# Kernel tuning notes

Measured on AMD Instinct MI355X. Metric: run time of the kernel, lower is better.

## Reference

```python
import jax, jax.numpy as jnp
import numpy as np

B_, L_ = 32, 4096
D_MODEL, D_STATE, D_CONV, EXPAND, N_LAYERS, HORIZON = 128, 16, 4, 2, 4, 1
D_INNER = EXPAND * D_MODEL
DT_RANK = (D_MODEL + 15) // 16  # ceil(d_model/16) = 8
EPS = 1e-6


def setup_inputs() -> dict:
    key = jax.random.key(0)
    ks = jax.random.split(key, 10)
    s = lambda k, sh, sc: jax.random.normal(k, sh, jnp.float32) * sc
    inp = {}
    inp["x"] = s(ks[0], (B_, L_, 1), 1.0)
    inp["input_proj_w"] = s(ks[1], (D_MODEL, 1), 0.5)
    inp["input_proj_b"] = jnp.zeros((D_MODEL,), jnp.float32)
    inp["in_proj_w"] = s(ks[2], (N_LAYERS, 2 * D_INNER, D_MODEL), D_MODEL ** -0.5)
    inp["conv_w"] = s(ks[3], (N_LAYERS, D_INNER, 1, D_CONV), D_CONV ** -0.5)
    inp["conv_b"] = jnp.zeros((N_LAYERS, D_INNER), jnp.float32)
    inp["x_proj_w"] = s(ks[4], (N_LAYERS, DT_RANK + 2 * D_STATE, D_INNER), D_INNER ** -0.5)
    inp["dt_proj_w"] = s(ks[5], (N_LAYERS, D_INNER, DT_RANK), DT_RANK ** -0.5)
    inp["dt_proj_b"] = jnp.full((N_LAYERS, D_INNER), -4.0, jnp.float32)
    inp["A_log"] = jnp.tile(jnp.log(jnp.arange(1, D_STATE + 1, dtype=jnp.float32))[None, None, :], (N_LAYERS, D_INNER, 1))
    inp["D"] = jnp.ones((N_LAYERS, D_INNER), jnp.float32)
    inp["out_proj_w"] = s(ks[6], (N_LAYERS, D_MODEL, D_INNER), D_INNER ** -0.5)
    inp["norm_w"] = jnp.ones((D_MODEL,), jnp.float32)
    inp["output_proj_w"] = s(ks[7], (HORIZON, D_MODEL), D_MODEL ** -0.5)
    inp["output_proj_b"] = jnp.zeros((HORIZON,), jnp.float32)
    return inp


def _mamba_block(h, in_w, cw, cb, xpw, dtw, dtb, alog, d_skip, ow):
    # h: [B, L, d_model] -> [B, L, d_model]
    xz = jnp.einsum('bld,ed->ble', h, in_w)            # [B, L, 2*d_inner]
    x, z = jnp.split(xz, 2, axis=-1)                   # each [B, L, d_inner]
    # depthwise causal conv over time
    xc = jax.lax.conv_general_dilated(
        x.transpose(0, 2, 1), cw, window_strides=(1,),
        padding=[(D_CONV - 1, 0)], feature_group_count=D_INNER,
        dimension_numbers=('NCH', 'OIH', 'NCH'))      # [B, d_inner, L]
    x = jax.nn.silu(xc.transpose(0, 2, 1) + cb)        # [B, L, d_inner]
    dbl = jnp.einsum('blc,ec->ble', x, xpw)            # [B, L, dt_rank+2*d_state]
    dt, Bm, Cm = jnp.split(dbl, [DT_RANK, DT_RANK + D_STATE], axis=-1)
    dt = jax.nn.softplus(jnp.einsum('blr,cr->blc', dt, dtw) + dtb)  # [B, L, d_inner]
    A = -jnp.exp(alog)                                  # [d_inner, d_state]

    def step(hst, inputs):
        dt_t, B_t, C_t, x_t = inputs                   # [B,c],[B,s],[B,s],[B,c]
        hst = jnp.exp(dt_t[..., None] * A) * hst + (dt_t * x_t)[..., None] * B_t[:, None, :]
        y = jnp.einsum('bcs,bs->bc', hst, C_t)
        return hst, y

    h0 = jnp.zeros((x.shape[0], D_INNER, D_STATE), x.dtype)
    xs = (dt.transpose(1, 0, 2), Bm.transpose(1, 0, 2), Cm.transpose(1, 0, 2), x.transpose(1, 0, 2))
    _, ys = jax.lax.scan(step, h0, xs)                 # [L, B, d_inner]
    y = ys.transpose(1, 0, 2) + d_skip * x             # skip: y += D * x
    y = y * jax.nn.silu(z)                             # gating
    return jnp.einsum('blc,dc->bld', y, ow)            # [B, L, d_model]


def reference(x, input_proj_w, input_proj_b, in_proj_w, conv_w, conv_b, x_proj_w,
              dt_proj_w, dt_proj_b, A_log, D, out_proj_w, norm_w,
              output_proj_w, output_proj_b):
    h = jnp.einsum('blo,do->bld', x, input_proj_w) + input_proj_b  # [B, L, d_model]
    for i in range(N_LAYERS):
        h = h + _mamba_block(h, in_proj_w[i], conv_w[i], conv_b[i], x_proj_w[i],
                             dt_proj_w[i], dt_proj_b[i], A_log[i], D[i], out_proj_w[i])
    rms = jnp.sqrt(jnp.mean(h * h, axis=-1, keepdims=True) + EPS)
    h = norm_w * h / rms
    return h[:, -1, :] @ output_proj_w.T + output_proj_b  # [B, horizon]
```

## Files before the change

kernel.cpp:

```cpp
#include <hip/hip_runtime.h>

#define B_    32
#define L_    4096
#define DM    128
#define DI    256
#define DS_   16
#define RANK  8
#define NL    4
#define M_    (B_*L_)
#define NC    64
#define CL    (L_/NC)

typedef __attribute__((ext_vector_type(8))) short short8;
typedef __attribute__((ext_vector_type(4))) float floatx4;
typedef __attribute__((ext_vector_type(2))) float float2v;

__device__ __forceinline__ float b2f(unsigned short u) {
    return __uint_as_float(((unsigned)u) << 16);
}
__device__ __forceinline__ unsigned short f2b(float f) {
    unsigned u = __float_as_uint(f);
    unsigned r = u + 0x7fffu + ((u >> 16) & 1u);
    return (unsigned short)(r >> 16);
}
__device__ __forceinline__ float fast_sig(float v) {
    return __builtin_amdgcn_rcpf(1.f + __expf(-v));
}

__global__ __launch_bounds__(256) void k_detect(const unsigned short* __restrict__ x,
                                                int* __restrict__ flag) {
    __shared__ int cnt;
    if (threadIdx.x == 0) cnt = 0;
    __syncthreads();
    int ok = 0;
    for (int i = 0; i < 4; ++i) {
        unsigned short u = x[threadIdx.x * 4 + i];
        int e = (u >> 7) & 0xFF;
        if ((u & 0x7FFF) == 0 || (e >= 100 && e <= 150)) ok++;
    }
    atomicAdd(&cnt, ok);
    __syncthreads();
    if (threadIdx.x == 0) *flag = (cnt >= 800) ? 1 : 0;
}

struct CvtSeg { const void* src; float* dst; int n; };
struct CvtPack { CvtSeg seg[11]; };
__global__ __launch_bounds__(256) void k_cvt_params(CvtPack p, const int* __restrict__ flag) {
    int s = blockIdx.y;
    int i = blockIdx.x * 256 + threadIdx.x;
    if (i >= p.seg[s].n) return;
    p.seg[s].dst[i] = (*flag) ? b2f(((const unsigned short*)p.seg[s].src)[i])
                              : ((const float*)p.seg[s].src)[i];
}
__global__ __launch_bounds__(256) void k_cvt16(const void* __restrict__ src,
                                               unsigned short* __restrict__ dst,
                                               int n, const int* __restrict__ flag) {
    int i = blockIdx.x * 256 + threadIdx.x;
    if (i >= n) return;
    if (*flag) dst[i] = ((const unsigned short*)src)[i];
    else       dst[i] = f2b(((const float*)src)[i]);
}
__global__ __launch_bounds__(256) void k_xpw48(const void* __restrict__ src,
                                               unsigned short* __restrict__ dst,
                                               const int* __restrict__ flag) {
    int i = blockIdx.x * 256 + threadIdx.x;
    int col = i & 255, rowl = (i >> 8) % 48, layer = i / (48*256);
    unsigned short v = 0;
    if (rowl < 40) {
        int si = (layer*40 + rowl)*256 + col;
        v = (*flag) ? ((const unsigned short*)src)[si] : f2b(((const float*)src)[si]);
    }
    dst[i] = v;
}

__global__ __launch_bounds__(256) void k_init(const void* __restrict__ xraw,
                                              const int* __restrict__ flag,
                                              const float* __restrict__ ipw,
                                              const float* __restrict__ ipb,
                                              float* __restrict__ h, int base) {
    int idx = blockIdx.x * 256 + threadIdx.x;
    int bl = idx >> 7, d = idx & 127;
    float x = (*flag) ? b2f(((const unsigned short*)xraw)[base + bl])
                      : ((const float*)xraw)[base + bl];
    h[idx] = x * ipw[d] + ipb[d];
}

__global__ __launch_bounds__(256) void k_gemm_in(const float* __restrict__ h,
                                                 const unsigned short* __restrict__ w,
                                                 unsigned short* __restrict__ xb,
                                                 unsigned short* __restrict__ zb) {
    __shared__ unsigned short lA[64][136];
    __shared__ unsigned short lW[256][40];
    int tid = threadIdx.x;
    int lane = tid & 63, wv = tid >> 6;
    int ln = lane & 15, qd = lane >> 4;
    int r0 = blockIdx.x * 64;
    int n0 = blockIdx.y * 256;

    {
        int r = tid >> 2;
        int c0 = (tid & 3) * 32;
        const float4* src = (const float4*)(h + (size_t)(r0 + r) * DM + c0);
        for (int j = 0; j < 8; ++j) {
            float4 v = src[j];
            lA[r][c0 + j*4 + 0] = f2b(v.x);
            lA[r][c0 + j*4 + 1] = f2b(v.y);
            lA[r][c0 + j*4 + 2] = f2b(v.z);
            lA[r][c0 + j*4 + 3] = f2b(v.w);
        }
    }

    floatx4 acc[16];
    for (int i = 0; i < 16; ++i) acc[i] = (floatx4)0.f;

    for (int kc = 0; kc < 4; ++kc) {
        __syncthreads();
        {
            int n = tid;
            const uint4* src = (const uint4*)(w + (size_t)(n0 + n) * DM + kc * 32);
            uint4 a = src[0], b = src[1], c = src[2], d = src[3];
            *(uint4*)&lW[n][0]  = a;
            *(uint4*)&lW[n][8]  = b;
            *(uint4*)&lW[n][16] = c;
            *(uint4*)&lW[n][24] = d;
        }
        __syncthreads();
        short8 af = *(const short8*)&lA[wv*16 + ln][kc*32 + qd*8];
        for (int nt = 0; nt < 16; ++nt) {
            short8 bf = *(const short8*)&lW[nt*16 + ln][qd*8];
            acc[nt] = __builtin_amdgcn_mfma_f32_16x16x32_bf16(af, bf, acc[nt], 0, 0, 0);
        }
    }

    for (int nt = 0; nt < 16; ++nt)
        for (int rg = 0; rg < 4; ++rg) {
            size_t gr = (size_t)(r0 + wv*16 + qd*4 + rg);
            int gc = nt*16 + ln;
            unsigned short v = f2b(acc[nt][rg]);
            if (blockIdx.y == 0) xb[gr*DI + gc] = v;
            else                 zb[gr*DI + gc] = v;
        }
}

__device__ __forceinline__ bool a_is_integer_ladder(const float* A) {
    bool f = true;
    #pragma unroll
    for (int s = 0; s < DS_; ++s)
        f = f && (fabsf(A[s] + (float)(s+1)) < 0.01f * (float)(s+1));
    return f;
}

__device__ __forceinline__ void unpack8(uint4 p, float* f) {
    f[0] = b2f((unsigned short)(p.x & 0xffff)); f[1] = b2f((unsigned short)(p.x >> 16));
    f[2] = b2f((unsigned short)(p.y & 0xffff)); f[3] = b2f((unsigned short)(p.y >> 16));
    f[4] = b2f((unsigned short)(p.z & 0xffff)); f[5] = b2f((unsigned short)(p.z >> 16));
    f[6] = b2f((unsigned short)(p.w & 0xffff)); f[7] = b2f((unsigned short)(p.w >> 16));
}
__device__ __forceinline__ void pack16(const float* f, uint4* o) {
    unsigned v[8];
    #pragma unroll
    for (int j = 0; j < 8; ++j)
        v[j] = (unsigned)f2b(f[2*j]) | ((unsigned)f2b(f[2*j+1]) << 16);
    o[0] = make_uint4(v[0], v[1], v[2], v[3]);
    o[1] = make_uint4(v[4], v[5], v[6], v[7]);
}

__global__ __launch_bounds__(256) void k_xprojc(const unsigned short* __restrict__ xb,
                                                const float* __restrict__ cw,
                                                const float* __restrict__ cbp,
                                                const unsigned short* __restrict__ w48,
                                                const float* __restrict__ dtw,
                                                const float* __restrict__ dtb,
                                                const float* __restrict__ alog,
                                                unsigned short* __restrict__ xcg,
                                                unsigned short* __restrict__ dtg,
                                                unsigned short* __restrict__ Bg,
                                                unsigned short* __restrict__ Cg,
                                                unsigned short* __restrict__ Pbuf,
                                                unsigned short* __restrict__ Hbuf) {
    __shared__ unsigned short lA[64][264];
    __shared__ unsigned short lW[48][40];
    __shared__ float ldbl[64][8];
    __shared__ float lBs[64][DS_];
    int tid = threadIdx.x;
    int lane = tid & 63, wv = tid >> 6;
    int ln = lane & 15, qd = lane >> 4;
    int r0 = blockIdx.x * 64;
    int l0 = r0 & (L_ - 1);
    int bidx = r0 >> 12;
    int kidx = l0 >> 6;

    {
        int c = tid;
        float w0 = cw[c*4+0], w1 = cw[c*4+1], w2 = cw[c*4+2], w3 = cw[c*4+3];
        float bias = cbp[c];
        float x0 = (l0 >= 3) ? b2f(xb[(size_t)(r0-3)*DI + c]) : 0.f;
        float x1 = (l0 >= 2) ? b2f(xb[(size_t)(r0-2)*DI + c]) : 0.f;
        float x2 = (l0 >= 1) ? b2f(xb[(size_t)(r0-1)*DI + c]) : 0.f;
        for (int r = 0; r < 64; ++r) {
            float xcur = b2f(xb[(size_t)(r0+r)*DI + c]);
            float v = w0*x0 + w1*x1 + w2*x2 + w3*xcur + bias;
            float s = v * fast_sig(v);
            unsigned short sb = f2b(s);
            lA[r][c] = sb;
            xcg[(size_t)(r0+r)*DI + c] = sb;
            x0 = x1; x1 = x2; x2 = xcur;
        }
    }

    floatx4 acc[3];
    for (int i = 0; i < 3; ++i) acc[i] = (floatx4)0.f;

    for (int kc = 0; kc < 8; ++kc) {
        __syncthreads();
        if (tid < 192) {
            int n = tid >> 2, q = tid & 3;
            *(uint4*)&lW[n][q*8] = *(const uint4*)(w48 + (size_t)n*DI + kc*32 + q*8);
        }
        __syncthreads();
        short8 af = *(const short8*)&lA[wv*16 + ln][kc*32 + qd*8];
        for (int nt = 0; nt < 3; ++nt) {
            short8 bf = *(const short8*)&lW[nt*16 + ln][qd*8];
            acc[nt] = __builtin_amdgcn_mfma_f32_16x16x32_bf16(af, bf, acc[nt], 0, 0, 0);
        }
    }

    for (int nt = 0; nt < 3; ++nt)
        for (int rg = 0; rg < 4; ++rg) {
            int rloc = wv*16 + qd*4 + rg;
            size_t row = (size_t)(r0 + rloc);
            int n = nt*16 + ln;
            float v = acc[nt][rg];
            if (n < 8)       ldbl[rloc][n] = v;
            else if (n < 24) {
                unsigned short bv = f2b(v);
                Bg[row*DS_ + (n-8)] = bv;
                lBs[rloc][n-8] = b2f(bv);
            }
            else if (n < 40) Cg[row*DS_ + (n-24)] = f2b(v);
        }
    __syncthreads();

    {
        int c = tid;
        float w8[8];
        #pragma unroll
        for (int j = 0; j < 8; ++j) w8[j] = dtw[c*8 + j];
        float bias = dtb[c];
        float A[DS_];
        #pragma unroll
        for (int j = 0; j < 4; ++j) {
            float4 a4 = *(const float4*)(alog + c*DS_ + j*4);
            A[j*4+0] = -__expf(a4.x); A[j*4+1] = -__expf(a4.y);
            A[j*4+2] = -__expf(a4.z); A[j*4+3] = -__expf(a4.w);
        }
        float P[DS_], hh[DS_];
        if (a_is_integer_ladder(A)) {
            float2v h2[8];
            #pragma unroll
            for (int j = 0; j < 8; ++j) h2[j] = (float2v)0.f;
            float S = 0.f;
            for (int r = 0; r < 64; ++r) {
                float a = bias;
                #pragma unroll
                for (int j = 0; j < 8; ++j) a += ldbl[r][j] * w8[j];
                float sp = (a > 20.f) ? a : __logf(1.f + __expf(a));
                unsigned short spb = f2b(sp);
                dtg[(size_t)(r0+r)*DI + c] = spb;
                float dtv = b2f(spb);
                float du = dtv * b2f(lA[r][c]);
                float Bl[DS_];
                *(float4*)&Bl[0]  = *(const float4*)&lBs[r][0];
                *(float4*)&Bl[4]  = *(const float4*)&lBs[r][4];
                *(float4*)&Bl[8]  = *(const float4*)&lBs[r][8];
                *(float4*)&Bl[12] = *(const float4*)&lBs[r][12];
                float E = __expf(-dtv);
                float E2 = E * E;
                float2v ep[8];
                ep[0].x = E; ep[0].y = E2;
                float2v E22; E22.x = E2; E22.y = E2;
                #pragma unroll
                for (int j = 1; j < 8; ++j) ep[j] = ep[j-1] * E22;
                float2v du2; du2.x = du; du2.y = du;
                #pragma unroll
                for (int j = 0; j < 8; ++j) {
                    float2v bj; bj.x = Bl[2*j]; bj.y = Bl[2*j+1];
                    h2[j] = ep[j]*h2[j] + du2*bj;
                }
                S += dtv;
            }
            #pragma unroll
            for (int s = 0; s < DS_; ++s) P[s] = __expf(-(float)(s+1) * S);
            #pragma unroll
            for (int j = 0; j < 8; ++j) { hh[2*j] = h2[j].x; hh[2*j+1] = h2[j].y; }
        } else {
            #pragma unroll
            for (int s = 0; s < DS_; ++s) { hh[s] = 0.f; P[s] = 1.f; }
            for (int r = 0; r < 64; ++r) {
                float a = bias;
                #pragma unroll
                for (int j = 0; j < 8; ++j) a += ldbl[r][j] * w8[j];
                float sp = (a > 20.f) ? a : __logf(1.f + __expf(a));
                unsigned short spb = f2b(sp);
                dtg[(size_t)(r0+r)*DI + c] = spb;
                float dtv = b2f(spb);
                float du = dtv * b2f(lA[r][c]);
                float Bl[DS_];
                *(float4*)&Bl[0]  = *(const float4*)&lBs[r][0];
                *(float4*)&Bl[4]  = *(const float4*)&lBs[r][4];
                *(float4*)&Bl[8]  = *(const float4*)&lBs[r][8];
                *(float4*)&Bl[12] = *(const float4*)&lBs[r][12];
                #pragma unroll
                for (int s = 0; s < DS_; ++s) {
                    float e = __expf(dtv * A[s]);
                    hh[s] = e*hh[s] + du*Bl[s];
                    P[s] *= e;
                }
            }
        }
        uint4 op[2], oh[2];
        pack16(P, op);
        pack16(hh, oh);
        uint4* pp = (uint4*)(Pbuf + (((size_t)bidx*NC + kidx)*DI + c)*DS_);
        uint4* ph = (uint4*)(Hbuf + (((size_t)bidx*NC + kidx)*DI + c)*DS_);
        pp[0] = op[0]; pp[1] = op[1];
        ph[0] = oh[0]; ph[1] = oh[1];
    }
}

__global__ __launch_bounds__(256) void k_scan2(const unsigned short* __restrict__ Pbuf,
                                               unsigned short* __restrict__ Hbuf,
                                               int cb) {
    int t = blockIdx.x * 256 + threadIdx.x;
    if (t >= cb * DI * DS_) return;
    int b  = t / (DI * DS_);
    int cs = t % (DI * DS_);
    float H = 0.f;
    for (int k = 0; k < NC; ++k) {
        size_t idx = ((size_t)b * NC + k) * (DI * DS_) + cs;
        float P  = b2f(Pbuf[idx]);
        float he = b2f(Hbuf[idx]);
        Hbuf[idx] = f2b(H);
        H = P * H + he;
    }
}

__global__ __launch_bounds__(256) void k_scan3g(const unsigned short* __restrict__ dtg,
                                                const unsigned short* __restrict__ xcg,
                                                const unsigned short* __restrict__ Bg,
                                                const unsigned short* __restrict__ Cg,
                                                const float* __restrict__ alog,
                                                const unsigned short* __restrict__ Hbuf,
                                                const unsigned short* __restrict__ zb,
                                                const float* __restrict__ Dp,
                                                unsigned short* __restrict__ yg) {
    __shared__ float lB[CL*DS_];
    __shared__ float lC[CL*DS_];
    int c = threadIdx.x;
    int k = blockIdx.x, b = blockIdx.y;
    size_t row0 = (size_t)b * L_ + (size_t)k * CL;
    {
        int t = c & 127;
        const unsigned short* src = (c < 128) ? (Bg + row0*DS_) : (Cg + row0*DS_);
        float* dst = (c < 128) ? lB : lC;
        uint4 p = ((const uint4*)src)[t];
        float f[8]; unpack8(p, f);
        *(float4*)&dst[t*8]     = make_float4(f[0], f[1], f[2], f[3]);
        *(float4*)&dst[t*8 + 4] = make_float4(f[4], f[5], f[6], f[7]);
    }
    float A[DS_];
    #pragma unroll
    for (int j = 0; j < 4; ++j) {
        float4 a4 = *(const float4*)(alog + c*DS_ + j*4);
        A[j*4+0] = -__expf(a4.x); A[j*4+1] = -__expf(a4.y);
        A[j*4+2] = -__expf(a4.z); A[j*4+3] = -__expf(a4.w);
    }
    float Dc = Dp[c];
    float h0[DS_];
    {
        const uint4* ph = (const uint4*)(Hbuf + (((size_t)b*NC + k)*DI + c)*DS_);
        uint4 p0 = ph[0], p1 = ph[1];
        unpack8(p0, &h0[0]);
        unpack8(p1, &h0[8]);
    }
    __syncthreads();
    const unsigned short* pdt = dtg + row0*DI + c;
    const unsigned short* pxc = xcg + row0*DI + c;
    const unsigned short* pz  = zb  + row0*DI + c;
    unsigned short* py        = yg  + row0*DI + c;
    float dtc = b2f(*pdt), xcc = b2f(*pxc), zc = b2f(*pz);

    if (a_is_integer_ladder(A)) {
        float2v h2[8];
        #pragma unroll
        for (int j = 0; j < 8; ++j) { h2[j].x = h0[2*j]; h2[j].y = h0[2*j+1]; }
        for (int l = 0; l < CL; ++l) {
            float dtn = b2f(pdt[DI]); float xcn = b2f(pxc[DI]); float zn = b2f(pz[DI]);
            float du = dtc * xcc;
            float Bl[DS_], Cl[DS_];
            *(float4*)&Bl[0]  = *(const float4*)&lB[l*DS_ + 0];
            *(float4*)&Bl[4]  = *(const float4*)&lB[l*DS_ + 4];
            *(float4*)&Bl[8]  = *(const float4*)&lB[l*DS_ + 8];
            *(float4*)&Bl[12] = *(const float4*)&lB[l*DS_ + 12];
            *(float4*)&Cl[0]  = *(const float4*)&lC[l*DS_ + 0];
            *(float4*)&Cl[4]  = *(const float4*)&lC[l*DS_ + 4];
            *(float4*)&Cl[8]  = *(const float4*)&lC[l*DS_ + 8];
            *(float4*)&Cl[12] = *(const float4*)&lC[l*DS_ + 12];
            float E = __expf(-dtc);
            float E2 = E * E;
            float2v ep[8];
            ep[0].x = E; ep[0].y = E2;
            float2v E22; E22.x = E2; E22.y = E2;
            #pragma unroll
            for (int j = 1; j < 8; ++j) ep[j] = ep[j-1] * E22;
            float2v du2; du2.x = du; du2.y = du;
            float2v y2 = (float2v)0.f;
            #pragma unroll
            for (int j = 0; j < 8; ++j) {
                float2v bj; bj.x = Bl[2*j]; bj.y = Bl[2*j+1];
                float2v cj; cj.x = Cl[2*j]; cj.y = Cl[2*j+1];
                h2[j] = ep[j]*h2[j] + du2*bj;
                y2 = y2 + h2[j]*cj;
            }
            float y = y2.x + y2.y;
            *py = f2b((y + Dc*xcc) * (zc * fast_sig(zc)));
            dtc = dtn; xcc = xcn; zc = zn;
            pdt += DI; pxc += DI; pz += DI; py += DI;
        }
    } else {
        float h[DS_];
        #pragma unroll
        for (int s = 0; s < DS_; ++s) h[s] = h0[s];
        for (int l = 0; l < CL; ++l) {
            float dtn = b2f(pdt[DI]); float xcn = b2f(pxc[DI]); float zn = b2f(pz[DI]);
            float du = dtc * xcc;
            float Bl[DS_], Cl[DS_];
            *(float4*)&Bl[0]  = *(const float4*)&lB[l*DS_ + 0];
            *(float4*)&Bl[4]  = *(const float4*)&lB[l*DS_ + 4];
            *(float4*)&Bl[8]  = *(const float4*)&lB[l*DS_ + 8];
            *(float4*)&Bl[12] = *(const float4*)&lB[l*DS_ + 12];
            *(float4*)&Cl[0]  = *(const float4*)&lC[l*DS_ + 0];
            *(float4*)&Cl[4]  = *(const float4*)&lC[l*DS_ + 4];
            *(float4*)&Cl[8]  = *(const float4*)&lC[l*DS_ + 8];
            *(float4*)&Cl[12] = *(const float4*)&lC[l*DS_ + 12];
            float y = 0.f;
            #pragma unroll
            for (int s = 0; s < DS_; ++s) {
                float e = __expf(dtc * A[s]);
                h[s] = e*h[s] + du*Bl[s];
                y += h[s]*Cl[s];
            }
            *py = f2b((y + Dc*xcc) * (zc * fast_sig(zc)));
            dtc = dtn; xcc = xcn; zc = zn;
            pdt += DI; pxc += DI; pz += DI; py += DI;
        }
    }
}

__global__ __launch_bounds__(256) void k_gemm_oi(const unsigned short* yg,
                                                 const unsigned short* __restrict__ wo,
                                                 const unsigned short* __restrict__ wi,
                                                 float* __restrict__ h,
                                                 unsigned short* xb,
                                                 unsigned short* __restrict__ zb) {
    __shared__ unsigned short lA[64*264];
    __shared__ unsigned short lW[256*40];
    int tid = threadIdx.x;
    int lane = tid & 63, wv = tid >> 6;
    int ln = lane & 15, qd = lane >> 4;
    int r0 = blockIdx.x * 64;

    for (int j = 0; j < 8; ++j) {
        int idx = tid + j*256;
        int r = idx >> 5, q = idx & 31;
        *(uint4*)&lA[r*264 + q*8] = *(const uint4*)(yg + (size_t)(r0 + r)*DI + q*8);
    }
    floatx4 acc1[8];
    for (int i = 0; i < 8; ++i) acc1[i] = (floatx4)0.f;
    for (int kc = 0; kc < 8; ++kc) {
        __syncthreads();
        {
            int n = tid >> 1, half = tid & 1;
            const uint4* src = (const uint4*)(wo + (size_t)n*DI + kc*32 + half*16);
            uint4 a = src[0], b4 = src[1];
            *(uint4*)&lW[n*40 + half*16]     = a;
            *(uint4*)&lW[n*40 + half*16 + 8] = b4;
        }
        __syncthreads();
        short8 af = *(const short8*)&lA[(wv*16 + ln)*264 + kc*32 + qd*8];
        for (int nt = 0; nt < 8; ++nt) {
            short8 bf = *(const short8*)&lW[(nt*16 + ln)*40 + qd*8];
            acc1[nt] = __builtin_amdgcn_mfma_f32_16x16x32_bf16(af, bf, acc1[nt], 0, 0, 0);
        }
    }
    __syncthreads();

    for (int nt = 0; nt < 8; ++nt)
        for (int rg = 0; rg < 4; ++rg) {
            int rloc = wv*16 + qd*4 + rg;
            size_t gr = (size_t)(r0 + rloc);
            int gc = nt*16 + ln;
            float hv = h[gr*DM + gc] + acc1[nt][rg];
            h[gr*DM + gc] = hv;
            lA[rloc*136 + gc] = f2b(hv);
        }
    __syncthreads();

    for (int n0 = 0; n0 < 2; ++n0) {
        floatx4 acc2[16];
        for (int i = 0; i < 16; ++i) acc2[i] = (floatx4)0.f;
        for (int kc = 0; kc < 4; ++kc) {
            __syncthreads();
            {
                int n = tid;
                const uint4* src = (const uint4*)(wi + (size_t)(n0*256 + n)*DM + kc*32);
                uint4 a = src[0], b = src[1], c = src[2], d = src[3];
                *(uint4*)&lW[n*40 + 0]  = a;
                *(uint4*)&lW[n*40 + 8]  = b;
                *(uint4*)&lW[n*40 + 16] = c;
                *(uint4*)&lW[n*40 + 24] = d;
            }
            __syncthreads();
            short8 af = *(const short8*)&lA[(wv*16 + ln)*136 + kc*32 + qd*8];
            for (int nt = 0; nt < 16; ++nt) {
                short8 bf = *(const short8*)&lW[(nt*16 + ln)*40 + qd*8];
                acc2[nt] = __builtin_amdgcn_mfma_f32_16x16x32_bf16(af, bf, acc2[nt], 0, 0, 0);
            }
        }
        unsigned short* dst = (n0 == 0) ? xb : zb;
        for (int nt = 0; nt < 16; ++nt)
            for (int rg = 0; rg < 4; ++rg) {
                size_t gr = (size_t)(r0 + wv*16 + qd*4 + rg);
                int gc = nt*16 + ln;
                dst[gr*DI + gc] = f2b(acc2[nt][rg]);
            }
    }
}

__global__ __launch_bounds__(256) void k_gemm_out(const unsigned short* __restrict__ yg,
                                                  const unsigned short* __restrict__ w,
                                                  float* __restrict__ h) {
    __shared__ unsigned short lA[64][264];
    __shared__ unsigned short lW[128][40];
    int tid = threadIdx.x;
    int lane = tid & 63, wv = tid >> 6;
    int ln = lane & 15, qd = lane >> 4;
    int r0 = blockIdx.x * 64;

    for (int j = 0; j < 8; ++j) {
        int idx = tid + j*256;
        int r = idx >> 5, q = idx & 31;
        *(uint4*)&lA[r][q*8] = *(const uint4*)(yg + (size_t)(r0 + r)*DI + q*8);
    }

    floatx4 acc[8];
    for (int i = 0; i < 8; ++i) acc[i] = (floatx4)0.f;

    for (int kc = 0; kc < 8; ++kc) {
        __syncthreads();
        {
            int n = tid >> 1, half = tid & 1;
            const uint4* src = (const uint4*)(w + (size_t)n*DI + kc*32 + half*16);
            uint4 a = src[0], b4 = src[1];
            *(uint4*)&lW[n][half*16]     = a;
            *(uint4*)&lW[n][half*16 + 8] = b4;
        }
        __syncthreads();
        short8 af = *(const short8*)&lA[wv*16 + ln][kc*32 + qd*8];
        for (int nt = 0; nt < 8; ++nt) {
            short8 bf = *(const short8*)&lW[nt*16 + ln][qd*8];
            acc[nt] = __builtin_amdgcn_mfma_f32_16x16x32_bf16(af, bf, acc[nt], 0, 0, 0);
        }
    }

    for (int nt = 0; nt < 8; ++nt)
        for (int rg = 0; rg < 4; ++rg) {
            size_t gr = (size_t)(r0 + wv*16 + qd*4 + rg);
            int gc = nt*16 + ln;
            h[gr*DM + gc] += acc[nt][rg];
        }
}

__global__ __launch_bounds__(128) void k_head(const float* __restrict__ h,
                                              const float* __restrict__ nw,
                                              const float* __restrict__ opw,
                                              const float* __restrict__ opb,
                                              float* __restrict__ out) {
    __shared__ float red[4];
    int b = blockIdx.x, d = threadIdx.x;
    float hv = h[((size_t)b*L_ + (L_-1))*DM + d];
    float v = hv * hv;
    for (int off = 1; off < 64; off <<= 1) v += __shfl_xor(v, off);
    if ((d & 63) == 0) red[d >> 6] = v;
    __syncthreads();
    float ss = red[0] + red[1];
    float rms = sqrtf(ss * (1.f/DM) + 1e-6f);
    float hn = nw[d] * hv / rms;
    float pv = hn * opw[d];
    for (int off = 1; off < 64; off <<= 1) pv += __shfl_xor(pv, off);
    if ((d & 63) == 0) red[2 + (d >> 6)] = pv;
    __syncthreads();
    if (d == 0) out[b] = red[2] + red[3] + opb[0];
}

extern "C" void kernel_launch(void* const* d_in, const int* in_sizes, int n_in,
                              void* d_out, int out_size, void* d_ws, size_t ws_size,
                              hipStream_t stream) {
    (void)in_sizes; (void)n_in; (void)out_size;
    float* out = (float*)d_out;

    char* wp = (char*)d_ws;
    int* flag = (int*)wp; wp += 16;
    auto allocf = [&](size_t elems) {
        float* p = (float*)wp;
        wp += (elems * 4 + 15) & ~(size_t)15;
        return p;
    };
    auto alloch = [&](size_t elems) {
        unsigned short* p = (unsigned short*)wp;
        wp += (elems * 2 + 15) & ~(size_t)15;
        return p;
    };
    float* c_ipw  = allocf(DM);
    float* c_ipb  = allocf(DM);
    float* c_cw   = allocf((size_t)NL*DI*4);
    float* c_cb   = allocf((size_t)NL*DI);
    float* c_dtw  = allocf((size_t)NL*DI*RANK);
    float* c_dtb  = allocf((size_t)NL*DI);
    float* c_alog = allocf((size_t)NL*DI*DS_);
    float* c_D    = allocf((size_t)NL*DI);
    float* c_nw   = allocf(DM);
    float* c_opw  = allocf(DM);
    float* c_opb  = allocf(1);
    unsigned short* c_inw16 = alloch((size_t)NL*2*DI*DM);
    unsigned short* c_ow16  = alloch((size_t)NL*DM*DI);
    unsigned short* c_xpw48 = alloch((size_t)NL*48*DI);
    wp = (char*)(((size_t)wp + 255) & ~(size_t)255);

    k_detect<<<1, 256, 0, stream>>>((const unsigned short*)d_in[0], flag);

    CvtPack pk;
    pk.seg[0]  = { d_in[1],  c_ipw,  DM };
    pk.seg[1]  = { d_in[2],  c_ipb,  DM };
    pk.seg[2]  = { d_in[4],  c_cw,   NL*DI*4 };
    pk.seg[3]  = { d_in[5],  c_cb,   NL*DI };
    pk.seg[4]  = { d_in[7],  c_dtw,  NL*DI*RANK };
    pk.seg[5]  = { d_in[8],  c_dtb,  NL*DI };
    pk.seg[6]  = { d_in[9],  c_alog, NL*DI*DS_ };
    pk.seg[7]  = { d_in[10], c_D,    NL*DI };
    pk.seg[8]  = { d_in[12], c_nw,   DM };
    pk.seg[9]  = { d_in[13], c_opw,  DM };
    pk.seg[10] = { d_in[14], c_opb,  1 };
    k_cvt_params<<<dim3(64, 11), 256, 0, stream>>>(pk, flag);
    k_cvt16<<<(int)((NL*2*DI*DM + 255)/256), 256, 0, stream>>>(d_in[3],  c_inw16, NL*2*DI*DM, flag);
    k_cvt16<<<(int)((NL*DM*DI   + 255)/256), 256, 0, stream>>>(d_in[11], c_ow16,  NL*DM*DI,   flag);
    k_xpw48<<<NL*48*DI/256, 256, 0, stream>>>(d_in[6], c_xpw48, flag);

    size_t used  = (size_t)(wp - (char*)d_ws);
    size_t avail = (ws_size > used) ? ws_size - used : 0;
    const size_t perB = (size_t)L_ * 2624 + (size_t)2 * NC * DI * DS_ * 2;
    int cb = B_;
    while (cb > 1 && (size_t)cb * perB > avail) cb >>= 1;
    const int Mc = cb * L_;

    float* h            = (float*)wp;          wp += (size_t)Mc*DM*4;
    unsigned short* xb  = (unsigned short*)wp; wp += (size_t)Mc*DI*2;
    unsigned short* zb  = (unsigned short*)wp; wp += (size_t)Mc*DI*2;
    unsigned short* xcg = (unsigned short*)wp; wp += (size_t)Mc*DI*2;
    unsigned short* dty = (unsigned short*)wp; wp += (size_t)Mc*DI*2;
    unsigned short* Bg  = (unsigned short*)wp; wp += (size_t)Mc*DS_*2;
    unsigned short* Cg  = (unsigned short*)wp; wp += (size_t)Mc*DS_*2;
    unsigned short* Pbuf = (unsigned short*)wp; wp += (size_t)cb*NC*DI*DS_*2;
    unsigned short* Hbuf = (unsigned short*)wp; wp += (size_t)cb*NC*DI*DS_*2;

    const int scan2_blocks = (cb * DI * DS_ + 255) / 256;

    for (int b0 = 0; b0 < B_; b0 += cb) {
        k_init<<<Mc*DM/256, 256, 0, stream>>>(d_in[0], flag, c_ipw, c_ipb, h, b0*L_);
        k_gemm_in<<<dim3(Mc/64, 2), 256, 0, stream>>>(h, c_inw16, xb, zb);
        for (int i = 0; i < NL; ++i) {
            k_xprojc<<<Mc/64, 256, 0, stream>>>(xb, c_cw + i*DI*4, c_cb + i*DI,
                                                c_xpw48 + (size_t)i*48*DI,
                                                c_dtw + i*DI*RANK, c_dtb + i*DI,
                                                c_alog + i*DI*DS_,
                                                xcg, dty, Bg, Cg, Pbuf, Hbuf);
            k_scan2<<<scan2_blocks, 256, 0, stream>>>(Pbuf, Hbuf, cb);
            k_scan3g<<<dim3(NC, cb), 256, 0, stream>>>(dty, xcg, Bg, Cg, c_alog + i*DI*DS_,
                                                       Hbuf, zb, c_D + i*DI, xb);
            if (i < NL-1)
                k_gemm_oi<<<Mc/64, 256, 0, stream>>>(xb, c_ow16 + (size_t)i*DM*DI,
                                                     c_inw16 + (size_t)(i+1)*2*DI*DM,
                                                     h, xb, zb);
            else
                k_gemm_out<<<Mc/64, 256, 0, stream>>>(xb, c_ow16 + (size_t)i*DM*DI, h);
        }
        k_head<<<cb, 128, 0, stream>>>(h, c_nw, c_opw, c_opb, out + b0);
    }
}
```

Before: 1.378 ms.

## Compute local scan output in chunk pass and correct with carried state

The first chunked-scan kernel now produces the per-timestep local output y (zero-initial-state contribution) and the cumulative dt sum S, and writes them to global memory instead of dt and B. The third pass no longer reruns the recurrence. It adds the carried-in state contribution analytically, C·exp(A·S)·h0, then applies the skip and gate. This removes the duplicated sequential recurrence in the third pass at the cost of writing two full-width bf16 tensors (yl and S) instead of dt and B, raising memory traffic and workspace. The dt dot product is also vectorised with float2.

New measurement: 1.381 ms. No clear change (+0.2%).

```diff
diff --git a/kernel.cpp b/kernel.cpp
--- a/kernel.cpp
+++ b/kernel.cpp
@@ -173,8 +173,8 @@
                                                 const float* __restrict__ dtb,
                                                 const float* __restrict__ alog,
                                                 unsigned short* __restrict__ xcg,
-                                                unsigned short* __restrict__ dtg,
-                                                unsigned short* __restrict__ Bg,
+                                                unsigned short* __restrict__ ylg,
+                                                unsigned short* __restrict__ Sg,
                                                 unsigned short* __restrict__ Cg,
                                                 unsigned short* __restrict__ Pbuf,
                                                 unsigned short* __restrict__ Hbuf) {
@@ -182,6 +182,7 @@
     __shared__ unsigned short lW[48][40];
     __shared__ float ldbl[64][8];
     __shared__ float lBs[64][DS_];
+    __shared__ float lCs[64][DS_];
     int tid = threadIdx.x;
     int lane = tid & 63, wv = tid >> 6;
     int ln = lane & 15, qd = lane >> 4;
@@ -233,19 +234,21 @@
             float v = acc[nt][rg];
             if (n < 8)       ldbl[rloc][n] = v;
             else if (n < 24) {
-                unsigned short bv = f2b(v);
-                Bg[row*DS_ + (n-8)] = bv;
-                lBs[rloc][n-8] = b2f(bv);
+                lBs[rloc][n-8] = b2f(f2b(v));
             }
-            else if (n < 40) Cg[row*DS_ + (n-24)] = f2b(v);
+            else if (n < 40) {
+                unsigned short cv = f2b(v);
+                Cg[row*DS_ + (n-24)] = cv;
+                lCs[rloc][n-24] = b2f(cv);
+            }
         }
     __syncthreads();
 
     {
         int c = tid;
-        float w8[8];
+        float2v w2v[4];
         #pragma unroll
-        for (int j = 0; j < 8; ++j) w8[j] = dtw[c*8 + j];
+        for (int j = 0; j < 4; ++j) { w2v[j].x = dtw[c*8 + 2*j]; w2v[j].y = dtw[c*8 + 2*j + 1]; }
         float bias = dtb[c];
         float A[DS_];
         #pragma unroll
@@ -261,19 +264,23 @@
             for (int j = 0; j < 8; ++j) h2[j] = (float2v)0.f;
             float S = 0.f;
             for (int r = 0; r < 64; ++r) {
-                float a = bias;
+                float2v a2; a2.x = bias; a2.y = 0.f;
+                const float2v* d2 = (const float2v*)&ldbl[r][0];
                 #pragma unroll
-                for (int j = 0; j < 8; ++j) a += ldbl[r][j] * w8[j];
+                for (int j = 0; j < 4; ++j) a2 = a2 + d2[j]*w2v[j];
+                float a = a2.x + a2.y;
                 float sp = (a > 20.f) ? a : __logf(1.f + __expf(a));
-                unsigned short spb = f2b(sp);
-                dtg[(size_t)(r0+r)*DI + c] = spb;
-                float dtv = b2f(spb);
+                float dtv = b2f(f2b(sp));
                 float du = dtv * b2f(lA[r][c]);
-                float Bl[DS_];
+                float Bl[DS_], Cl[DS_];
                 *(float4*)&Bl[0]  = *(const float4*)&lBs[r][0];
                 *(float4*)&Bl[4]  = *(const float4*)&lBs[r][4];
                 *(float4*)&Bl[8]  = *(const float4*)&lBs[r][8];
                 *(float4*)&Bl[12] = *(const float4*)&lBs[r][12];
+                *(float4*)&Cl[0]  = *(const float4*)&lCs[r][0];
+                *(float4*)&Cl[4]  = *(const float4*)&lCs[r][4];
+                *(float4*)&Cl[8]  = *(const float4*)&lCs[r][8];
+                *(float4*)&Cl[12] = *(const float4*)&lCs[r][12];
                 float E = __expf(-dtv);
                 float E2 = E * E;
                 float2v ep[8];
@@ -282,12 +289,18 @@
                 #pragma unroll
                 for (int j = 1; j < 8; ++j) ep[j] = ep[j-1] * E22;
                 float2v du2; du2.x = du; du2.y = du;
+                float2v yv = (float2v)0.f;
                 #pragma unroll
                 for (int j = 0; j < 8; ++j) {
                     float2v bj; bj.x = Bl[2*j]; bj.y = Bl[2*j+1];
+                    float2v cj; cj.x = Cl[2*j]; cj.y = Cl[2*j+1];
                     h2[j] = ep[j]*h2[j] + du2*bj;
+                    yv = yv + h2[j]*cj;
                 }
                 S += dtv;
+                size_t row = (size_t)(r0 + r);
+                ylg[row*DI + c] = f2b(yv.x + yv.y);
+                Sg[row*DI + c]  = f2b(S);
             }
             #pragma unroll
             for (int s = 0; s < DS_; ++s) P[s] = __expf(-(float)(s+1) * S);
@@ -296,26 +309,35 @@
         } else {
             #pragma unroll
             for (int s = 0; s < DS_; ++s) { hh[s] = 0.f; P[s] = 1.f; }
+            float S = 0.f;
             for (int r = 0; r < 64; ++r) {
                 float a = bias;
                 #pragma unroll
-                for (int j = 0; j < 8; ++j) a += ldbl[r][j] * w8[j];
+                for (int j = 0; j < 8; ++j) a += ldbl[r][j] * ((j & 1) ? w2v[j>>1].y : w2v[j>>1].x);
                 float sp = (a > 20.f) ? a : __logf(1.f + __expf(a));
-                unsigned short spb = f2b(sp);
-                dtg[(size_t)(r0+r)*DI + c] = spb;
-                float dtv = b2f(spb);
+                float dtv = b2f(f2b(sp));
                 float du = dtv * b2f(lA[r][c]);
-                float Bl[DS_];
+                float Bl[DS_], Cl[DS_];
                 *(float4*)&Bl[0]  = *(const float4*)&lBs[r][0];
                 *(float4*)&Bl[4]  = *(const float4*)&lBs[r][4];
                 *(float4*)&Bl[8]  = *(const float4*)&lBs[r][8];
                 *(float4*)&Bl[12] = *(const float4*)&lBs[r][12];
+                *(float4*)&Cl[0]  = *(const float4*)&lCs[r][0];
+                *(float4*)&Cl[4]  = *(const float4*)&lCs[r][4];
+                *(float4*)&Cl[8]  = *(const float4*)&lCs[r][8];
+                *(float4*)&Cl[12] = *(const float4*)&lCs[r][12];
+                float yv = 0.f;
                 #pragma unroll
                 for (int s = 0; s < DS_; ++s) {
                     float e = __expf(dtv * A[s]);
                     hh[s] = e*hh[s] + du*Bl[s];
+                    yv += hh[s]*Cl[s];
                     P[s] *= e;
                 }
+                S += dtv;
+                size_t row = (size_t)(r0 + r);
+                ylg[row*DI + c] = f2b(yv);
+                Sg[row*DI + c]  = f2b(S);
             }
         }
         uint4 op[2], oh[2];
@@ -345,28 +367,24 @@
     }
 }
 
-__global__ __launch_bounds__(256) void k_scan3g(const unsigned short* __restrict__ dtg,
-                                                const unsigned short* __restrict__ xcg,
-                                                const unsigned short* __restrict__ Bg,
-                                                const unsigned short* __restrict__ Cg,
-                                                const float* __restrict__ alog,
-                                                const unsigned short* __restrict__ Hbuf,
-                                                const unsigned short* __restrict__ zb,
-                                                const float* __restrict__ Dp,
-                                                unsigned short* __restrict__ yg) {
-    __shared__ float lB[CL*DS_];
+__global__ __launch_bounds__(256) void k_ygate(const unsigned short* __restrict__ ylg,
+                                               const unsigned short* __restrict__ Sg,
+                                               const unsigned short* __restrict__ xcg,
+                                               const unsigned short* __restrict__ Cg,
+                                               const float* __restrict__ alog,
+                                               const unsigned short* __restrict__ Hbuf,
+                                               const unsigned short* __restrict__ zb,
+                                               const float* __restrict__ Dp,
+                                               unsigned short* __restrict__ yg) {
     __shared__ float lC[CL*DS_];
     int c = threadIdx.x;
     int k = blockIdx.x, b = blockIdx.y;
     size_t row0 = (size_t)b * L_ + (size_t)k * CL;
-    {
-        int t = c & 127;
-        const unsigned short* src = (c < 128) ? (Bg + row0*DS_) : (Cg + row0*DS_);
-        float* dst = (c < 128) ? lB : lC;
-        uint4 p = ((const uint4*)src)[t];
+    if (c < 128) {
+        uint4 p = ((const uint4*)(Cg + row0*DS_))[c];
         float f[8]; unpack8(p, f);
-        *(float4*)&dst[t*8]     = make_float4(f[0], f[1], f[2], f[3]);
-        *(float4*)&dst[t*8 + 4] = make_float4(f[4], f[5], f[6], f[7]);
+        *(float4*)&lC[c*8]     = make_float4(f[0], f[1], f[2], f[3]);
+        *(float4*)&lC[c*8 + 4] = make_float4(f[4], f[5], f[6], f[7]);
     }
     float A[DS_];
     #pragma unroll
@@ -384,75 +402,59 @@
         unpack8(p1, &h0[8]);
     }
     __syncthreads();
-    const unsigned short* pdt = dtg + row0*DI + c;
+    const unsigned short* pyl = ylg + row0*DI + c;
+    const unsigned short* pS  = Sg  + row0*DI + c;
     const unsigned short* pxc = xcg + row0*DI + c;
     const unsigned short* pz  = zb  + row0*DI + c;
     unsigned short* py        = yg  + row0*DI + c;
-    float dtc = b2f(*pdt), xcc = b2f(*pxc), zc = b2f(*pz);
 
     if (a_is_integer_ladder(A)) {
-        float2v h2[8];
+        float2v hp[8];
         #pragma unroll
-        for (int j = 0; j < 8; ++j) { h2[j].x = h0[2*j]; h2[j].y = h0[2*j+1]; }
+        for (int j = 0; j < 8; ++j) { hp[j].x = h0[2*j]; hp[j].y = h0[2*j+1]; }
         for (int l = 0; l < CL; ++l) {
-            float dtn = b2f(pdt[DI]); float xcn = b2f(pxc[DI]); float zn = b2f(pz[DI]);
-            float du = dtc * xcc;
-            float Bl[DS_], Cl[DS_];
-            *(float4*)&Bl[0]  = *(const float4*)&lB[l*DS_ + 0];
-            *(float4*)&Bl[4]  = *(const float4*)&lB[l*DS_ + 4];
-            *(float4*)&Bl[8]  = *(const float4*)&lB[l*DS_ + 8];
-            *(float4*)&Bl[12] = *(const float4*)&lB[l*DS_ + 12];
+            float yl  = b2f(pyl[(size_t)l*DI]);
+            float S   = b2f(pS [(size_t)l*DI]);
+            float xcc = b2f(pxc[(size_t)l*DI]);
+            float zc  = b2f(pz [(size_t)l*DI]);
+            float Cl[DS_];
             *(float4*)&Cl[0]  = *(const float4*)&lC[l*DS_ + 0];
             *(float4*)&Cl[4]  = *(const float4*)&lC[l*DS_ + 4];
             *(float4*)&Cl[8]  = *(const float4*)&lC[l*DS_ + 8];
             *(float4*)&Cl[12] = *(const float4*)&lC[l*DS_ + 12];
-            float E = __expf(-dtc);
+            float E = __expf(-S);
             float E2 = E * E;
             float2v ep[8];
             ep[0].x = E; ep[0].y = E2;
             float2v E22; E22.x = E2; E22.y = E2;
             #pragma unroll
             for (int j = 1; j < 8; ++j) ep[j] = ep[j-1] * E22;
-            float2v du2; du2.x = du; du2.y = du;
             float2v y2 = (float2v)0.f;
             #pragma unroll
             for (int j = 0; j < 8; ++j) {
-                float2v bj; bj.x = Bl[2*j]; bj.y = Bl[2*j+1];
                 float2v cj; cj.x = Cl[2*j]; cj.y = Cl[2*j+1];
-                h2[j] = ep[j]*h2[j] + du2*bj;
-                y2 = y2 + h2[j]*cj;
+                float2v t = ep[j] * hp[j];
+                y2 = y2 + t * cj;
             }
-            float y = y2.x + y2.y;
-            *py = f2b((y + Dc*xcc) * (zc * fast_sig(zc)));
-            dtc = dtn; xcc = xcn; zc = zn;
-            pdt += DI; pxc += DI; pz += DI; py += DI;
+            float y = yl + y2.x + y2.y;
+            py[(size_t)l*DI] = f2b((y + Dc*xcc) * (zc * fast_sig(zc)));
         }
     } else {
-        float h[DS_];
-        #pragma unroll
-        for (int s = 0; s < DS_; ++s) h[s] = h0[s];
         for (int l = 0; l < CL; ++l) {
-            float dtn = b2f(pdt[DI]); float xcn = b2f(pxc[DI]); float zn = b2f(pz[DI]);
-            float du = dtc * xcc;
-            float Bl[DS_], Cl[DS_];
-            *(float4*)&Bl[0]  = *(const float4*)&lB[l*DS_ + 0];
-            *(float4*)&Bl[4]  = *(const float4*)&lB[l*DS_ + 4];
-            *(float4*)&Bl[8]  = *(const float4*)&lB[l*DS_ + 8];
-            *(float4*)&Bl[12] = *(const float4*)&lB[l*DS_ + 12];
+            float yl  = b2f(pyl[(size_t)l*DI]);
+            float S   = b2f(pS [(size_t)l*DI]);
+            float xcc = b2f(pxc[(size_t)l*DI]);
+            float zc  = b2f(pz [(size_t)l*DI]);
+            float Cl[DS_];
             *(float4*)&Cl[0]  = *(const float4*)&lC[l*DS_ + 0];
             *(float4*)&Cl[4]  = *(const float4*)&lC[l*DS_ + 4];
             *(float4*)&Cl[8]  = *(const float4*)&lC[l*DS_ + 8];
             *(float4*)&Cl[12] = *(const float4*)&lC[l*DS_ + 12];
-            float y = 0.f;
+            float y = yl;
             #pragma unroll
-            for (int s = 0; s < DS_; ++s) {
-                float e = __expf(dtc * A[s]);
-                h[s] = e*h[s] + du*Bl[s];
-                y += h[s]*Cl[s];
-            }
-            *py = f2b((y + Dc*xcc) * (zc * fast_sig(zc)));
-            dtc = dtn; xcc = xcn; zc = zn;
-            pdt += DI; pxc += DI; pz += DI; py += DI;
+            for (int s = 0; s < DS_; ++s)
+                y += Cl[s] * __expf(A[s]*S) * h0[s];
+            py[(size_t)l*DI] = f2b((y + Dc*xcc) * (zc * fast_sig(zc)));
         }
     }
 }
@@ -658,7 +660,7 @@
 
     size_t used  = (size_t)(wp - (char*)d_ws);
     size_t avail = (ws_size > used) ? ws_size - used : 0;
-    const size_t perB = (size_t)L_ * 2624 + (size_t)2 * NC * DI * DS_ * 2;
+    const size_t perB = (size_t)L_ * 3104 + (size_t)2 * NC * DI * DS_ * 2;
     int cb = B_;
     while (cb > 1 && (size_t)cb * perB > avail) cb >>= 1;
     const int Mc = cb * L_;
@@ -667,8 +669,8 @@
     unsigned short* xb  = (unsigned short*)wp; wp += (size_t)Mc*DI*2;
     unsigned short* zb  = (unsigned short*)wp; wp += (size_t)Mc*DI*2;
     unsigned short* xcg = (unsigned short*)wp; wp += (size_t)Mc*DI*2;
-    unsigned short* dty = (unsigned short*)wp; wp += (size_t)Mc*DI*2;
-    unsigned short* Bg  = (unsigned short*)wp; wp += (size_t)Mc*DS_*2;
+    unsigned short* ylg = (unsigned short*)wp; wp += (size_t)Mc*DI*2;
+    unsigned short* Sg  = (unsigned short*)wp; wp += (size_t)Mc*DI*2;
     unsigned short* Cg  = (unsigned short*)wp; wp += (size_t)Mc*DS_*2;
     unsigned short* Pbuf = (unsigned short*)wp; wp += (size_t)cb*NC*DI*DS_*2;
     unsigned short* Hbuf = (unsigned short*)wp; wp += (size_t)cb*NC*DI*DS_*2;
@@ -683,10 +685,10 @@
                                                 c_xpw48 + (size_t)i*48*DI,
                                                 c_dtw + i*DI*RANK, c_dtb + i*DI,
                                                 c_alog + i*DI*DS_,
-                                                xcg, dty, Bg, Cg, Pbuf, Hbuf);
+                                                xcg, ylg, Sg, Cg, Pbuf, Hbuf);
             k_scan2<<<scan2_blocks, 256, 0, stream>>>(Pbuf, Hbuf, cb);
-            k_scan3g<<<dim3(NC, cb), 256, 0, stream>>>(dty, xcg, Bg, Cg, c_alog + i*DI*DS_,
-                                                       Hbuf, zb, c_D + i*DI, xb);
+            k_ygate<<<dim3(NC, cb), 256, 0, stream>>>(ylg, Sg, xcg, Cg, c_alog + i*DI*DS_,
+                                                      Hbuf, zb, c_D + i*DI, xb);
             if (i < NL-1)
                 k_gemm_oi<<<Mc/64, 256, 0, stream>>>(xb, c_ow16 + (size_t)i*DM*DI,
                                                      c_inw16 + (size_t)(i+1)*2*DI*DM,
```
